# Kernel optimization log

Hardware: AMD Instinct MI355X
Metric: run time of the kernel (lower is better)

Reference implementation:

```python
import jax, jax.numpy as jnp
import numpy as np

N_AB = 8
L = 3
N_REF = 3
ANC = 0
M = 20
NV = N_AB
NQ = N_AB + N_REF + ANC  # 11
K = N_AB - L             # 5
DIM = 2 ** NQ            # 2048

# CNOT as (in_c, in_t, out_c, out_t); matches einsum 'bvf,fg->bvg' with f=(q1,q2) bits
CNOT4 = jnp.array([[1., 0, 0, 0],
                   [0, 1, 0, 0],
                   [0, 0, 0, 1],
                   [0, 0, 1, 0]], dtype=jnp.float32).reshape(2, 2, 2, 2)


def ry_mat(angle):
    c = jnp.cos(angle / 2.0)
    s = jnp.sin(angle / 2.0)
    # [[c, -s], [s, c]]; original contracts as state @ gate ('bvi,ij->bvj')
    return jnp.stack([jnp.stack([c, -s]), jnp.stack([s, c])])


def apply_1q(state, q, gate):
    # state: [b, 2^NQ]; qubit q is big-endian axis q of [2]*NQ view
    b = state.shape[0]
    t = state.reshape(b, 2 ** q, 2, -1)
    out = jnp.einsum('blir,ij->bljr', t, gate)
    return out.reshape(b, -1)


def apply_2q(state, q1, q2, gate4):
    # gate4: [2,2,2,2] with indices (in_q1, in_q2, out_q1, out_q2)
    b = state.shape[0]
    a, c = (q1, q2) if q1 < q2 else (q2, q1)
    t = state.reshape(b, 2 ** a, 2, 2 ** (c - a - 1), 2, -1)
    if q1 < q2:
        out = jnp.einsum('bxiyjz,ijkl->bxkylz', t, gate4)
    else:
        out = jnp.einsum('bxjyiz,ijkl->bxlykz', t, gate4)
    return out.reshape(b, -1)


def setup_inputs() -> dict:
    key = jax.random.key(0)
    k1, k2 = jax.random.split(key)
    x = jax.random.uniform(k1, (1024, 2 ** N_AB), dtype=jnp.float32)
    theta = jax.random.normal(k2, ((M + 1) * NV,), dtype=jnp.float32) * 0.08
    return {"x": x, "theta": theta}


def reference(x, theta):
    b = x.shape[0]
    # amplitude encode: state[:, i << (n_ref+anc)] = x[:, i]
    inds = np.arange(2 ** N_AB) << (N_REF + ANC)
    state = jnp.zeros((b, DIM), dtype=x.dtype).at[:, inds].set(x)
    pidx = 0
    for m in range(M):
        for q in range(NV):
            state = apply_1q(state, q, ry_mat(theta[pidx + q]))
        pidx += NV
        # cw_fixed ring: control q -> target (q+1) % NV
        for q in range(NV):
            state = apply_2q(state, q, (q + 1) % NV, CNOT4)
    for q in range(NV):
        state = apply_1q(state, q, ry_mat(theta[pidx + q]))
    # qubits: A = 0..K-1, B = K..K+L-1, Bp = rest (anc=0)
    t = state.reshape(b, 2 ** K, 2 ** L, 2 ** N_REF)
    probs_B = jnp.sum(t * t, axis=(1, 3))  # [b, 2^L]
    return probs_B
```

## Files before the change

### kernel.cpp

```cpp
#include <hip/hip_runtime.h>


namespace {

struct M8 { unsigned r[8]; };

constexpr M8 kI{{0x01,0x02,0x04,0x08,0x10,0x20,0x40,0x80}};
constexpr M8 kP{{0xFF,0xFE,0xFC,0xF8,0xF0,0xE0,0xC0,0x7F}};
constexpr M8 kQ{{0x03,0x06,0x0C,0x18,0x30,0x60,0xC1,0x81}};

constexpr M8 mul(const M8& A, const M8& B) {
  M8 C{{0,0,0,0,0,0,0,0}};
  for (int j = 0; j < 8; ++j) {
    unsigned by = 0;
    for (int b = 0; b < 8; ++b) by |= ((B.r[b] >> j) & 1u) << b;
    for (int b = 0; b < 8; ++b) {
      unsigned v = A.r[b] & by;
      v ^= v >> 4; v ^= v >> 2; v ^= v >> 1;
      C.r[b] |= (v & 1u) << j;
    }
  }
  return C;
}

constexpr bool eqI(const M8& A) {
  bool e = true;
  for (int b = 0; b < 8; ++b) e = e && (A.r[b] == (1u << b));
  return e;
}

struct Tables { unsigned Mm[21][8]; unsigned Rr[21][8]; bool ok; };

constexpr Tables build() {
  Tables t{};
  M8 T = kI, Ti = kI;
  bool ok = eqI(mul(kP, kQ)) && eqI(mul(kQ, kP));
  for (int m = 0; m <= 20; ++m) {
    ok = ok && eqI(mul(T, Ti));
    for (int b = 0; b < 8; ++b) {
      unsigned mm = 0;
      for (int k = 0; k < 8; ++k) mm |= ((Ti.r[k] >> b) & 1u) << k;
      t.Mm[m][b] = mm;
      t.Rr[m][b] = T.r[b];
    }
    T = mul(kP, T);
    Ti = mul(Ti, kQ);
  }
  t.ok = ok;
  return t;
}

constexpr Tables kT = build();
static_assert(kT.ok, "GF(2) inverse tracking failed");

constexpr int single_cost(int m, int a) {
  return (((kT.Mm[m][a] >> 2) != 0) ? 8 : 0) + 1;
}
constexpr int pair_cost(int m, int a, int b) {
  const unsigned LA = kT.Mm[m][a] >> 2, LB = kT.Mm[m][b] >> 2, LC = LA ^ LB;
  int c = 0;
  if (LA) ++c;
  if (LB && LB != LA) ++c;
  if (LC && LC != LA && LC != LB) ++c;
  return 8 * c + 1;
}

struct PlanCost { int n; int pa[8]; int pb[8]; int cost; };

constexpr PlanCost search(int m, unsigned used) {
  if (used == 0xFFu) {
    PlanCost r{0, {0,0,0,0,0,0,0,0}, {0,0,0,0,0,0,0,0}, 0};
    return r;
  }
  int a = 0;
  while ((used >> a) & 1u) ++a;
  PlanCost best = search(m, used | (1u << a));
  best.pa[best.n] = a; best.pb[best.n] = -1;
  best.n += 1; best.cost += single_cost(m, a);
  for (int b = a + 1; b < 8; ++b) {
    if ((used >> b) & 1u) continue;
    PlanCost sub = search(m, used | (1u << a) | (1u << b));
    const int c = sub.cost + pair_cost(m, a, b);
    if (c < best.cost) {
      sub.pa[sub.n] = a; sub.pb[sub.n] = b;
      sub.n += 1; sub.cost = c;
      best = sub;
    }
  }
  return best;
}

struct AllPlans { int nops[21]; int pa[21][8]; int pb[21][8]; };

constexpr AllPlans build_plans() {
  AllPlans ap{};
  for (int m = 0; m < 21; ++m) {
    const PlanCost pc = search(m, 0u);
    ap.nops[m] = pc.n;
    for (int k = 0; k < 8; ++k) {
      ap.pa[m][k] = (k < pc.n) ? pc.pa[k] : 0;
      ap.pb[m][k] = (k < pc.n) ? pc.pb[k] : -1;
    }
  }
  return ap;
}

constexpr AllPlans kPlans = build_plans();

constexpr bool plans_ok() {
  for (int m = 0; m < 21; ++m) {
    unsigned mask = 0; int cnt = 0;
    for (int k = 0; k < kPlans.nops[m]; ++k) {
      mask |= 1u << kPlans.pa[m][k]; ++cnt;
      if (kPlans.pb[m][k] >= 0) { mask |= 1u << kPlans.pb[m][k]; ++cnt; }
    }
    if (mask != 0xFFu || cnt != 8) return false;
  }
  return true;
}
static_assert(plans_ok(), "bad gate schedule");

__constant__ AllPlans dPlans = build_plans();

struct LaneSet { unsigned L[3]; };
constexpr LaneSet lane_set(unsigned a, unsigned b, unsigned c) {
  LaneSet r{{0,0,0}}; int n = 0;
  const unsigned v[3] = {a, b, c};
  for (int i = 0; i < 3; ++i) {
    if (!v[i]) continue;
    bool dup = false;
    for (int j = 0; j < n; ++j) if (r.L[j] == v[i]) dup = true;
    if (!dup) r.L[n++] = v[i];
  }
  return r;
}

template<unsigned RX, int IDX>
__device__ __forceinline__ float pick(const float (&s)[4], const float (&t0)[4],
                                      const float (&t1)[4], const float (&t2)[4], int j) {
  if constexpr (IDX == 0) return t0[j ^ (int)RX];
  else if constexpr (IDX == 1) return t1[j ^ (int)RX];
  else if constexpr (IDX == 2) return t2[j ^ (int)RX];
  else return s[j ^ (int)RX];
}

template<int m, int op>
__device__ __forceinline__ void do_op(int lane, const float4* __restrict__ ct4,
                                      float (&s)[4], float (&u)[4]) {
  constexpr int ga = kPlans.pa[m][op];
  constexpr int gb = kPlans.pb[m][op];
  constexpr unsigned MA = kT.Mm[m][ga];
  constexpr unsigned RA = kT.Rr[m][ga];
  constexpr unsigned LA = MA >> 2;
  const float4 k = ct4[m * 8 + op];

  if constexpr (gb < 0) {
    float tAs[4], tAu[4];
    #pragma unroll
    for (int j = 0; j < 4; ++j) {
      float ps = s[j ^ (int)(MA & 3u)];
      float pu = u[j ^ (int)(MA & 3u)];
      if constexpr (LA != 0) { ps = __shfl_xor(ps, (int)LA); pu = __shfl_xor(pu, (int)LA); }
      tAs[j] = ps; tAu[j] = pu;
    }
    const int sa = __popc((int)(RA >> 2) & lane) & 1;
    const float wa = sa ? -k.y : k.y;
    float ns[4], nu[4];
    #pragma unroll
    for (int j = 0; j < 4; ++j) {
      const int pj = __popc((int)(RA & 3u) & j) & 1;
      const float va = pj ? -wa : wa;
      ns[j] = fmaf(va, tAs[j], k.x * s[j]);
      nu[j] = fmaf(va, tAu[j], k.x * u[j]);
    }
    #pragma unroll
    for (int j = 0; j < 4; ++j) { s[j] = ns[j]; u[j] = nu[j]; }
  } else {
    constexpr unsigned MB = kT.Mm[m][gb], MC = MA ^ MB;
    constexpr unsigned RB = kT.Rr[m][gb];
    constexpr unsigned LB = MB >> 2, LC = MC >> 2;
    constexpr LaneSet LS = lane_set(LA, LB, LC);
    constexpr unsigned L1 = LS.L[0], L2 = LS.L[1], L3 = LS.L[2];
    constexpr int iA = (LA == 0) ? -1 : (LA == L1 ? 0 : (LA == L2 ? 1 : 2));
    constexpr int iB = (LB == 0) ? -1 : (LB == L1 ? 0 : (LB == L2 ? 1 : 2));
    constexpr int iC = (LC == 0) ? -1 : (LC == L1 ? 0 : (LC == L2 ? 1 : 2));

    float b1s[4], b1u[4], b2s[4], b2u[4], b3s[4], b3u[4];
    if constexpr (L1 != 0) {
      #pragma unroll
      for (int j = 0; j < 4; ++j) { b1s[j] = __shfl_xor(s[j], (int)L1); b1u[j] = __shfl_xor(u[j], (int)L1); }
    }
    if constexpr (L2 != 0) {
      #pragma unroll
      for (int j = 0; j < 4; ++j) { b2s[j] = __shfl_xor(s[j], (int)L2); b2u[j] = __shfl_xor(u[j], (int)L2); }
    }
    if constexpr (L3 != 0) {
      #pragma unroll
      for (int j = 0; j < 4; ++j) { b3s[j] = __shfl_xor(s[j], (int)L3); b3u[j] = __shfl_xor(u[j], (int)L3); }
    }

    const int sa = __popc((int)(RA >> 2) & lane) & 1;
    const int sb = __popc((int)(RB >> 2) & lane) & 1;
    const float wa = sa ? -k.y : k.y;
    const float wb = sb ? -k.z : k.z;
    const float wc = (sa ^ sb) ? -k.w : k.w;

    float ns[4], nu[4];
    #pragma unroll
    for (int j = 0; j < 4; ++j) {
      const int pa_ = __popc((int)(RA & 3u) & j) & 1;
      const int pb_ = __popc((int)(RB & 3u) & j) & 1;
      const float vA = pa_ ? -wa : wa;
      const float vB = pb_ ? -wb : wb;
      const float vC = (pa_ ^ pb_) ? -wc : wc;
      ns[j] = fmaf(vC, pick<MC & 3u, iC>(s, b1s, b2s, b3s, j),
              fmaf(vB, pick<MB & 3u, iB>(s, b1s, b2s, b3s, j),
              fmaf(vA, pick<MA & 3u, iA>(s, b1s, b2s, b3s, j), k.x * s[j])));
      nu[j] = fmaf(vC, pick<MC & 3u, iC>(u, b1u, b2u, b3u, j),
              fmaf(vB, pick<MB & 3u, iB>(u, b1u, b2u, b3u, j),
              fmaf(vA, pick<MA & 3u, iA>(u, b1u, b2u, b3u, j), k.x * u[j])));
    }
    #pragma unroll
    for (int j = 0; j < 4; ++j) { s[j] = ns[j]; u[j] = nu[j]; }
  }
}

template<int m, int op>
__device__ __forceinline__ void run_ops(int lane, const float4* __restrict__ ct4,
                                        float (&s)[4], float (&u)[4]) {
  if constexpr (op < kPlans.nops[m]) {
    do_op<m, op>(lane, ct4, s, u);
    run_ops<m, op + 1>(lane, ct4, s, u);
  }
}

template<int m>
__device__ __forceinline__ void run_all(int lane, const float4* __restrict__ ct4,
                                        float (&s)[4], float (&u)[4]) {
  if constexpr (m <= 20) {
    run_ops<m, 0>(lane, ct4, s, u);
    run_all<m + 1>(lane, ct4, s, u);
  }
}

}

__global__ __launch_bounds__(128) void qae_kernel(const float* __restrict__ x,
                                                  const float* __restrict__ theta,
                                                  float* __restrict__ out) {
  __shared__ float4 ct4[168];
  const int t = threadIdx.x;
  for (int tt = t; tt < 168; tt += 128) {
    const int m = tt >> 3, op = tt & 7;
    if (op < dPlans.nops[m]) {
      const int ga = dPlans.pa[m][op], gb = dPlans.pb[m][op];
      float sA, cA;
      sincosf(theta[m * 8 + (7 - ga)] * 0.5f, &sA, &cA);
      if (gb >= 0) {
        float sB, cB;
        sincosf(theta[m * 8 + (7 - gb)] * 0.5f, &sB, &cB);
        ct4[tt] = make_float4(cA * cB, sA * cB, cA * sB, sA * sB);
      } else {
        ct4[tt] = make_float4(cA, sA, 0.f, 0.f);
      }
    }
  }
  __syncthreads();

  const int lane = t & 63;
  const int wave = t >> 6;
  const int b0 = blockIdx.x * 4 + wave * 2;

  const float4 xv0 = *reinterpret_cast<const float4*>(x + (size_t)b0 * 256 + lane * 4);
  const float4 xv1 = *reinterpret_cast<const float4*>(x + (size_t)(b0 + 1) * 256 + lane * 4);
  float s[4] = {xv0.x, xv0.y, xv0.z, xv0.w};
  float u[4] = {xv1.x, xv1.y, xv1.z, xv1.w};

  run_all<0>(lane, ct4, s, u);

  constexpr unsigned R0 = kT.Rr[20][0], R1 = kT.Rr[20][1], R2 = kT.Rr[20][2];
  const int q0 = __popc((int)(R0 >> 2) & lane) & 1;
  const int q1 = __popc((int)(R1 >> 2) & lane) & 1;
  const int q2 = __popc((int)(R2 >> 2) & lane) & 1;

  float accS[8], accU[8];
  #pragma unroll
  for (int B = 0; B < 8; ++B) { accS[B] = 0.f; accU[B] = 0.f; }
  #pragma unroll
  for (int j = 0; j < 4; ++j) {
    const int bj = (q0 ^ (__popc((int)(R0 & 3u) & j) & 1))
                 | ((q1 ^ (__popc((int)(R1 & 3u) & j) & 1)) << 1)
                 | ((q2 ^ (__popc((int)(R2 & 3u) & j) & 1)) << 2);
    const float ps = s[j] * s[j];
    const float pu = u[j] * u[j];
    #pragma unroll
    for (int B = 0; B < 8; ++B) {
      accS[B] += (bj == B) ? ps : 0.f;
      accU[B] += (bj == B) ? pu : 0.f;
    }
  }
  #pragma unroll
  for (int mm = 1; mm < 64; mm <<= 1) {
    #pragma unroll
    for (int B = 0; B < 8; ++B) {
      accS[B] += __shfl_xor(accS[B], mm);
      accU[B] += __shfl_xor(accU[B], mm);
    }
  }
  if (lane == 0) {
    float4* o = reinterpret_cast<float4*>(out + (size_t)b0 * 8);
    o[0] = make_float4(accS[0], accS[1], accS[2], accS[3]);
    o[1] = make_float4(accS[4], accS[5], accS[6], accS[7]);
  } else if (lane == 1) {
    float4* o = reinterpret_cast<float4*>(out + (size_t)(b0 + 1) * 8);
    o[0] = make_float4(accU[0], accU[1], accU[2], accU[3]);
    o[1] = make_float4(accU[4], accU[5], accU[6], accU[7]);
  }
}

extern "C" void kernel_launch(void* const* d_in, const int* in_sizes, int n_in,
                              void* d_out, int out_size, void* d_ws, size_t ws_size,
                              hipStream_t stream) {
  const float* x = (const float*)d_in[0];
  const float* theta = (const float*)d_in[1];
  float* out = (float*)d_out;
  qae_kernel<<<256, 128, 0, stream>>>(x, theta, out);
}
```

Before: 22.57 us.

## Replace ds_bpermute shuffles with DPP/permlane swaps and one sample per wave

Cross-lane exchanges that used __shfl_xor, which on AMD goes through LDS bpermute, are replaced by DPP row permutes and v_permlane16/32_swap instructions. The gate-pairing plan is re-searched with a cost model tuned to those instruction counts, using a bitmask DP instead of recursion. Each wave now handles one batch sample instead of two, and blocks grow to 256 threads to keep the grid the same, which trades per-wave ILP for more waves. The inline asm with s_nop padding and the xor trick around permlane swaps depend on exact gfx950 semantics.

```diff
diff --git a/kernel.cpp b/kernel.cpp
--- a/kernel.cpp
+++ b/kernel.cpp
@@ -53,41 +53,22 @@
 constexpr Tables kT = build();
 static_assert(kT.ok, "GF(2) inverse tracking failed");
 
-constexpr int single_cost(int m, int a) {
-  return (((kT.Mm[m][a] >> 2) != 0) ? 8 : 0) + 1;
-}
+constexpr int dppc(unsigned l) {
+  if (l == 0u) return 0;
+  if (l == 1u || l == 2u || l == 3u || l == 7u || l == 8u || l == 15u) return 1;
+  return 2;
+}
+constexpr int xc(unsigned L) {
+  return ((L & 32u) ? 3 : 0) + ((L & 16u) ? 3 : 0) + dppc(L & 15u);
+}
+
+constexpr int single_cost(int m, int a) { return 4 * xc(kT.Mm[m][a] >> 2) + 10; }
 constexpr int pair_cost(int m, int a, int b) {
   const unsigned LA = kT.Mm[m][a] >> 2, LB = kT.Mm[m][b] >> 2, LC = LA ^ LB;
-  int c = 0;
-  if (LA) ++c;
-  if (LB && LB != LA) ++c;
-  if (LC && LC != LA && LC != LB) ++c;
-  return 8 * c + 1;
-}
-
-struct PlanCost { int n; int pa[8]; int pb[8]; int cost; };
-
-constexpr PlanCost search(int m, unsigned used) {
-  if (used == 0xFFu) {
-    PlanCost r{0, {0,0,0,0,0,0,0,0}, {0,0,0,0,0,0,0,0}, 0};
-    return r;
-  }
-  int a = 0;
-  while ((used >> a) & 1u) ++a;
-  PlanCost best = search(m, used | (1u << a));
-  best.pa[best.n] = a; best.pb[best.n] = -1;
-  best.n += 1; best.cost += single_cost(m, a);
-  for (int b = a + 1; b < 8; ++b) {
-    if ((used >> b) & 1u) continue;
-    PlanCost sub = search(m, used | (1u << a) | (1u << b));
-    const int c = sub.cost + pair_cost(m, a, b);
-    if (c < best.cost) {
-      sub.pa[sub.n] = a; sub.pb[sub.n] = b;
-      sub.n += 1; sub.cost = c;
-      best = sub;
-    }
-  }
-  return best;
+  int c = xc(LA);
+  if (LB != LA) c += xc(LB);
+  if (LC != LA && LC != LB) c += xc(LC);
+  return 4 * c + 18;
 }
 
 struct AllPlans { int nops[21]; int pa[21][8]; int pb[21][8]; };
@@ -95,12 +76,40 @@
 constexpr AllPlans build_plans() {
   AllPlans ap{};
   for (int m = 0; m < 21; ++m) {
-    const PlanCost pc = search(m, 0u);
-    ap.nops[m] = pc.n;
-    for (int k = 0; k < 8; ++k) {
-      ap.pa[m][k] = (k < pc.n) ? pc.pa[k] : 0;
-      ap.pb[m][k] = (k < pc.n) ? pc.pb[k] : -1;
-    }
+    int sc[8] = {};
+    int pc[8][8] = {};
+    for (int a = 0; a < 8; ++a) {
+      sc[a] = single_cost(m, a);
+      for (int b = a + 1; b < 8; ++b) pc[a][b] = pair_cost(m, a, b);
+    }
+    int dp[256] = {};
+    int chb[256] = {};
+    for (int used = 254; used >= 0; --used) {
+      int a = 0;
+      while ((used >> a) & 1) ++a;
+      int best = dp[used | (1 << a)] + sc[a];
+      int bb = -1;
+      for (int b = a + 1; b < 8; ++b) {
+        if ((used >> b) & 1) continue;
+        const int c = dp[used | (1 << a) | (1 << b)] + pc[a][b];
+        if (c < best) { best = c; bb = b; }
+      }
+      dp[used] = best;
+      chb[used] = bb;
+    }
+    int used = 0, n = 0;
+    while (used != 255) {
+      int a = 0;
+      while ((used >> a) & 1) ++a;
+      const int bb = chb[used];
+      ap.pa[m][n] = a;
+      ap.pb[m][n] = bb;
+      used |= 1 << a;
+      if (bb >= 0) used |= 1 << bb;
+      ++n;
+    }
+    ap.nops[m] = n;
+    for (int k = n; k < 8; ++k) { ap.pa[m][k] = 0; ap.pb[m][k] = -1; }
   }
   return ap;
 }
@@ -121,6 +130,66 @@
 static_assert(plans_ok(), "bad gate schedule");
 
 __constant__ AllPlans dPlans = build_plans();
+
+constexpr int dpp1(unsigned l) {
+  return l == 1u ? 0xB1 : l == 2u ? 0x4E : l == 3u ? 0x1B :
+         l == 7u ? 0x141 : l == 8u ? 0x128 : l == 15u ? 0x140 : -1;
+}
+constexpr unsigned fstep(unsigned l) {
+  switch (l) {
+    case 4u: return 3u;  case 5u: return 2u;  case 6u: return 1u;
+    case 9u: return 1u;  case 10u: return 2u; case 11u: return 3u;
+    case 12u: return 3u; case 13u: return 2u; case 14u: return 1u;
+  }
+  return 0u;
+}
+
+__device__ __forceinline__ int swap16(int x) {
+  int a, b;
+  asm volatile("v_mov_b32 %0, %2\n\t"
+               "v_mov_b32 %1, %2\n\t"
+               "s_nop 1\n\t"
+               "v_permlane16_swap_b32 %0, %1\n\t"
+               "s_nop 1"
+               : "=&v"(a), "=&v"(b) : "v"(x));
+  return a ^ b ^ x;
+}
+__device__ __forceinline__ int swap32(int x) {
+  int a, b;
+  asm volatile("v_mov_b32 %0, %2\n\t"
+               "v_mov_b32 %1, %2\n\t"
+               "s_nop 1\n\t"
+               "v_permlane32_swap_b32 %0, %1\n\t"
+               "s_nop 1"
+               : "=&v"(a), "=&v"(b) : "v"(x));
+  return a ^ b ^ x;
+}
+
+template<unsigned L>
+__device__ __forceinline__ float xshfl(float v, int lane) {
+  if constexpr (L == 0u) {
+    return v;
+  } else {
+    int x = __float_as_int(v);
+    constexpr unsigned low = L & 15u;
+    if constexpr (low != 0u) {
+      constexpr int c1 = dpp1(low);
+      if constexpr (c1 >= 0) {
+        x = __builtin_amdgcn_update_dpp(x, x, c1, 0xF, 0xF, false);
+      } else {
+        constexpr unsigned f = fstep(low);
+        constexpr int ca = dpp1(f);
+        constexpr int cb = dpp1(low ^ f);
+        x = __builtin_amdgcn_update_dpp(x, x, ca, 0xF, 0xF, false);
+        x = __builtin_amdgcn_update_dpp(x, x, cb, 0xF, 0xF, false);
+      }
+    }
+    if constexpr (L & 16u) x = swap16(x);
+    if constexpr (L & 32u) x = swap32(x);
+    (void)lane;
+    return __int_as_float(x);
+  }
+}
 
 struct LaneSet { unsigned L[3]; };
 constexpr LaneSet lane_set(unsigned a, unsigned b, unsigned c) {
@@ -145,39 +214,32 @@
 }
 
 template<int m, int op>
-__device__ __forceinline__ void do_op(int lane, const float4* __restrict__ ct4,
-                                      float (&s)[4], float (&u)[4]) {
+__device__ __forceinline__ void do_op(int lane, const float4* __restrict__ ct4, float (&s)[4]) {
   constexpr int ga = kPlans.pa[m][op];
   constexpr int gb = kPlans.pb[m][op];
   constexpr unsigned MA = kT.Mm[m][ga];
   constexpr unsigned RA = kT.Rr[m][ga];
   constexpr unsigned LA = MA >> 2;
   const float4 k = ct4[m * 8 + op];
+  const int sa = __popc((int)(RA >> 2) & lane) & 1;
 
   if constexpr (gb < 0) {
-    float tAs[4], tAu[4];
+    float tA[4];
+    #pragma unroll
+    for (int j = 0; j < 4; ++j) tA[j] = xshfl<LA>(s[j ^ (int)(MA & 3u)], lane);
+    const float wa = sa ? -k.y : k.y;
+    float ns[4];
     #pragma unroll
     for (int j = 0; j < 4; ++j) {
-      float ps = s[j ^ (int)(MA & 3u)];
-      float pu = u[j ^ (int)(MA & 3u)];
-      if constexpr (LA != 0) { ps = __shfl_xor(ps, (int)LA); pu = __shfl_xor(pu, (int)LA); }
-      tAs[j] = ps; tAu[j] = pu;
-    }
-    const int sa = __popc((int)(RA >> 2) & lane) & 1;
-    const float wa = sa ? -k.y : k.y;
-    float ns[4], nu[4];
-    #pragma unroll
-    for (int j = 0; j < 4; ++j) {
-      const int pj = __popc((int)(RA & 3u) & j) & 1;
-      const float va = pj ? -wa : wa;
-      ns[j] = fmaf(va, tAs[j], k.x * s[j]);
-      nu[j] = fmaf(va, tAu[j], k.x * u[j]);
-    }
-    #pragma unroll
-    for (int j = 0; j < 4; ++j) { s[j] = ns[j]; u[j] = nu[j]; }
+      const float va = (__popc((int)(RA & 3u) & j) & 1) ? -wa : wa;
+      ns[j] = fmaf(va, tA[j], k.x * s[j]);
+    }
+    #pragma unroll
+    for (int j = 0; j < 4; ++j) s[j] = ns[j];
   } else {
-    constexpr unsigned MB = kT.Mm[m][gb], MC = MA ^ MB;
-    constexpr unsigned RB = kT.Rr[m][gb];
+    constexpr int gb2 = (gb < 0) ? 0 : gb;
+    constexpr unsigned MB = kT.Mm[m][gb2], MC = MA ^ MB;
+    constexpr unsigned RB = kT.Rr[m][gb2];
     constexpr unsigned LB = MB >> 2, LC = MC >> 2;
     constexpr LaneSet LS = lane_set(LA, LB, LC);
     constexpr unsigned L1 = LS.L[0], L2 = LS.L[1], L3 = LS.L[2];
@@ -185,27 +247,26 @@
     constexpr int iB = (LB == 0) ? -1 : (LB == L1 ? 0 : (LB == L2 ? 1 : 2));
     constexpr int iC = (LC == 0) ? -1 : (LC == L1 ? 0 : (LC == L2 ? 1 : 2));
 
-    float b1s[4], b1u[4], b2s[4], b2u[4], b3s[4], b3u[4];
+    float b1[4], b2[4], b3[4];
     if constexpr (L1 != 0) {
       #pragma unroll
-      for (int j = 0; j < 4; ++j) { b1s[j] = __shfl_xor(s[j], (int)L1); b1u[j] = __shfl_xor(u[j], (int)L1); }
+      for (int j = 0; j < 4; ++j) b1[j] = xshfl<L1>(s[j], lane);
     }
     if constexpr (L2 != 0) {
       #pragma unroll
-      for (int j = 0; j < 4; ++j) { b2s[j] = __shfl_xor(s[j], (int)L2); b2u[j] = __shfl_xor(u[j], (int)L2); }
+      for (int j = 0; j < 4; ++j) b2[j] = xshfl<L2>(s[j], lane);
     }
     if constexpr (L3 != 0) {
       #pragma unroll
-      for (int j = 0; j < 4; ++j) { b3s[j] = __shfl_xor(s[j], (int)L3); b3u[j] = __shfl_xor(u[j], (int)L3); }
-    }
-
-    const int sa = __popc((int)(RA >> 2) & lane) & 1;
+      for (int j = 0; j < 4; ++j) b3[j] = xshfl<L3>(s[j], lane);
+    }
+
     const int sb = __popc((int)(RB >> 2) & lane) & 1;
     const float wa = sa ? -k.y : k.y;
     const float wb = sb ? -k.z : k.z;
     const float wc = (sa ^ sb) ? -k.w : k.w;
 
-    float ns[4], nu[4];
+    float ns[4];
     #pragma unroll
     for (int j = 0; j < 4; ++j) {
       const int pa_ = __popc((int)(RA & 3u) & j) & 1;
@@ -213,45 +274,46 @@
       const float vA = pa_ ? -wa : wa;
       const float vB = pb_ ? -wb : wb;
       const float vC = (pa_ ^ pb_) ? -wc : wc;
-      ns[j] = fmaf(vC, pick<MC & 3u, iC>(s, b1s, b2s, b3s, j),
-              fmaf(vB, pick<MB & 3u, iB>(s, b1s, b2s, b3s, j),
-              fmaf(vA, pick<MA & 3u, iA>(s, b1s, b2s, b3s, j), k.x * s[j])));
-      nu[j] = fmaf(vC, pick<MC & 3u, iC>(u, b1u, b2u, b3u, j),
-              fmaf(vB, pick<MB & 3u, iB>(u, b1u, b2u, b3u, j),
-              fmaf(vA, pick<MA & 3u, iA>(u, b1u, b2u, b3u, j), k.x * u[j])));
-    }
-    #pragma unroll
-    for (int j = 0; j < 4; ++j) { s[j] = ns[j]; u[j] = nu[j]; }
+      ns[j] = fmaf(vC, pick<MC & 3u, iC>(s, b1, b2, b3, j),
+              fmaf(vB, pick<MB & 3u, iB>(s, b1, b2, b3, j),
+              fmaf(vA, pick<MA & 3u, iA>(s, b1, b2, b3, j), k.x * s[j])));
+    }
+    #pragma unroll
+    for (int j = 0; j < 4; ++j) s[j] = ns[j];
   }
 }
 
 template<int m, int op>
-__device__ __forceinline__ void run_ops(int lane, const float4* __restrict__ ct4,
-                                        float (&s)[4], float (&u)[4]) {
+__device__ __forceinline__ void run_ops(int lane, const float4* __restrict__ ct4, float (&s)[4]) {
   if constexpr (op < kPlans.nops[m]) {
-    do_op<m, op>(lane, ct4, s, u);
-    run_ops<m, op + 1>(lane, ct4, s, u);
+    do_op<m, op>(lane, ct4, s);
+    run_ops<m, op + 1>(lane, ct4, s);
   }
 }
 
 template<int m>
-__device__ __forceinline__ void run_all(int lane, const float4* __restrict__ ct4,
-                                        float (&s)[4], float (&u)[4]) {
+__device__ __forceinline__ void run_all(int lane, const float4* __restrict__ ct4, float (&s)[4]) {
   if constexpr (m <= 20) {
-    run_ops<m, 0>(lane, ct4, s, u);
-    run_all<m + 1>(lane, ct4, s, u);
-  }
-}
-
-}
-
-__global__ __launch_bounds__(128) void qae_kernel(const float* __restrict__ x,
+    run_ops<m, 0>(lane, ct4, s);
+    run_all<m + 1>(lane, ct4, s);
+  }
+}
+
+template<unsigned MK>
+__device__ __forceinline__ void red_stage(float (&a)[8], int lane) {
+  #pragma unroll
+  for (int B = 0; B < 8; ++B) a[B] += xshfl<MK>(a[B], lane);
+}
+
+}
+
+__global__ __launch_bounds__(256) void qae_kernel(const float* __restrict__ x,
                                                   const float* __restrict__ theta,
                                                   float* __restrict__ out) {
   __shared__ float4 ct4[168];
   const int t = threadIdx.x;
-  for (int tt = t; tt < 168; tt += 128) {
-    const int m = tt >> 3, op = tt & 7;
+  if (t < 168) {
+    const int m = t >> 3, op = t & 7;
     if (op < dPlans.nops[m]) {
       const int ga = dPlans.pa[m][op], gb = dPlans.pb[m][op];
       float sA, cA;
@@ -259,62 +321,50 @@
       if (gb >= 0) {
         float sB, cB;
         sincosf(theta[m * 8 + (7 - gb)] * 0.5f, &sB, &cB);
-        ct4[tt] = make_float4(cA * cB, sA * cB, cA * sB, sA * sB);
+        ct4[t] = make_float4(cA * cB, sA * cB, cA * sB, sA * sB);
       } else {
-        ct4[tt] = make_float4(cA, sA, 0.f, 0.f);
+        ct4[t] = make_float4(cA, sA, 0.f, 0.f);
       }
     }
   }
   __syncthreads();
 
   const int lane = t & 63;
-  const int wave = t >> 6;
-  const int b0 = blockIdx.x * 4 + wave * 2;
-
-  const float4 xv0 = *reinterpret_cast<const float4*>(x + (size_t)b0 * 256 + lane * 4);
-  const float4 xv1 = *reinterpret_cast<const float4*>(x + (size_t)(b0 + 1) * 256 + lane * 4);
-  float s[4] = {xv0.x, xv0.y, xv0.z, xv0.w};
-  float u[4] = {xv1.x, xv1.y, xv1.z, xv1.w};
-
-  run_all<0>(lane, ct4, s, u);
+  const int b = blockIdx.x * 4 + (t >> 6);
+
+  const float4 xv = *reinterpret_cast<const float4*>(x + (size_t)b * 256 + lane * 4);
+  float s[4] = {xv.x, xv.y, xv.z, xv.w};
+
+  run_all<0>(lane, ct4, s);
 
   constexpr unsigned R0 = kT.Rr[20][0], R1 = kT.Rr[20][1], R2 = kT.Rr[20][2];
   const int q0 = __popc((int)(R0 >> 2) & lane) & 1;
   const int q1 = __popc((int)(R1 >> 2) & lane) & 1;
   const int q2 = __popc((int)(R2 >> 2) & lane) & 1;
 
-  float accS[8], accU[8];
+  float acc[8];
   #pragma unroll
-  for (int B = 0; B < 8; ++B) { accS[B] = 0.f; accU[B] = 0.f; }
+  for (int B = 0; B < 8; ++B) acc[B] = 0.f;
   #pragma unroll
   for (int j = 0; j < 4; ++j) {
     const int bj = (q0 ^ (__popc((int)(R0 & 3u) & j) & 1))
                  | ((q1 ^ (__popc((int)(R1 & 3u) & j) & 1)) << 1)
                  | ((q2 ^ (__popc((int)(R2 & 3u) & j) & 1)) << 2);
-    const float ps = s[j] * s[j];
-    const float pu = u[j] * u[j];
-    #pragma unroll
-    for (int B = 0; B < 8; ++B) {
-      accS[B] += (bj == B) ? ps : 0.f;
-      accU[B] += (bj == B) ? pu : 0.f;
-    }
-  }
-  #pragma unroll
-  for (int mm = 1; mm < 64; mm <<= 1) {
-    #pragma unroll
-    for (int B = 0; B < 8; ++B) {
-      accS[B] += __shfl_xor(accS[B], mm);
-      accU[B] += __shfl_xor(accU[B], mm);
-    }
-  }
+    const float pj = s[j] * s[j];
+    #pragma unroll
+    for (int B = 0; B < 8; ++B) acc[B] += (bj == B) ? pj : 0.f;
+  }
+  red_stage<1>(acc, lane);
+  red_stage<2>(acc, lane);
+  red_stage<4>(acc, lane);
+  red_stage<8>(acc, lane);
+  red_stage<16>(acc, lane);
+  red_stage<32>(acc, lane);
+
   if (lane == 0) {
-    float4* o = reinterpret_cast<float4*>(out + (size_t)b0 * 8);
-    o[0] = make_float4(accS[0], accS[1], accS[2], accS[3]);
-    o[1] = make_float4(accS[4], accS[5], accS[6], accS[7]);
-  } else if (lane == 1) {
-    float4* o = reinterpret_cast<float4*>(out + (size_t)(b0 + 1) * 8);
-    o[0] = make_float4(accU[0], accU[1], accU[2], accU[3]);
-    o[1] = make_float4(accU[4], accU[5], accU[6], accU[7]);
+    float4* o = reinterpret_cast<float4*>(out + (size_t)b * 8);
+    o[0] = make_float4(acc[0], acc[1], acc[2], acc[3]);
+    o[1] = make_float4(acc[4], acc[5], acc[6], acc[7]);
   }
 }
 
@@ -324,5 +374,5 @@
   const float* x = (const float*)d_in[0];
   const float* theta = (const float*)d_in[1];
   float* out = (float*)d_out;
-  qae_kernel<<<256, 128, 0, stream>>>(x, theta, out);
-}
+  qae_kernel<<<256, 256, 0, stream>>>(x, theta, out);
+}
```

New measurement: 24.30 us. +7.7%, slower.
